# Kernel tuning notes

Measured on AMD Instinct MI355X. Metric: run time of the kernel, lower is better.

Reference implementation:

```python
import jax, jax.numpy as jnp
import numpy as np

N_NODES = 100000
N_EDGES = 1600000
IN_DIM = 128
HID_DIM = 128
OUT_DIM = 64


def gcn_conv(x, W, b, edge_index):
    """GCNConv with add_self_loops, symmetric degree norm, add-aggregation.

    Math matches PyG: out[i] = sum_{(j,i) in E+selfloops} norm_ji * (x_j @ W) + b
    Since lin is linear and there is no edge_attr, we transform x once before
    the gather instead of per-edge (identical result, far less FLOPs/traffic).
    """
    n = x.shape[0]
    loop = jnp.arange(n, dtype=edge_index.dtype)
    row = jnp.concatenate([edge_index[0], loop])  # source nodes (x_j)
    col = jnp.concatenate([edge_index[1], loop])  # destination nodes
    # degree over destinations (includes self loops -> deg >= 1, no div by 0)
    deg = jax.ops.segment_sum(jnp.ones_like(col, dtype=x.dtype), col, num_segments=n)
    dinv = jax.lax.rsqrt(deg)
    norm = dinv[row] * dinv[col]  # [E+N]
    h = x @ W  # [N, out] transform once
    msg = norm[:, None] * h[row]  # [E+N, out] gathered per-edge messages
    out = jax.ops.segment_sum(msg, col, num_segments=n)  # scatter-add
    return out + b


def setup_inputs() -> dict:
    key = jax.random.key(0)
    k1, k2, k3, k4 = jax.random.split(key, 4)
    x = jax.random.normal(k1, (N_NODES, IN_DIM), dtype=jnp.float32)
    edge_index = jax.random.randint(k2, (2, N_EDGES), 0, N_NODES, dtype=jnp.int64)
    # glorot-ish init
    W1 = jax.random.normal(k3, (IN_DIM, HID_DIM), dtype=jnp.float32) * (2.0 / (IN_DIM + HID_DIM)) ** 0.5
    W2 = jax.random.normal(k4, (HID_DIM, OUT_DIM), dtype=jnp.float32) * (2.0 / (HID_DIM + OUT_DIM)) ** 0.5
    b1 = jnp.zeros((HID_DIM,), dtype=jnp.float32)
    b2 = jnp.zeros((OUT_DIM,), dtype=jnp.float32)
    return {"x": x, "edge_index": edge_index, "W1": W1, "b1": b1, "W2": W2, "b2": b2}


def reference(x, edge_index, W1, b1, W2, b2):
    # GCN.forward with prompt_type=None, pooling=False, eval mode (dropout is identity)
    h = gcn_conv(x, W1, b1, edge_index)
    h = jax.nn.relu(h)
    out = gcn_conv(h, W2, b2, edge_index)
    return out
```

## Files before the change

### kernel.cpp

```cpp
#include <hip/hip_runtime.h>


#define DIN 128
#define DHID 128
#define DOUT 64
#define ELLW 64
#define GPART 8
#define BPG 512

typedef __attribute__((ext_vector_type(4))) float f32x4;
typedef __attribute__((ext_vector_type(8))) short bf16x8;

__device__ __forceinline__ float bf2f(unsigned int u16) {
    return __uint_as_float(u16 << 16);
}
__device__ __forceinline__ unsigned short f2bf(float f) {
    unsigned int u = __float_as_uint(f);
    u += 0x7fffu + ((u >> 16) & 1u);
    return (unsigned short)(u >> 16);
}
__device__ __forceinline__ unsigned int pack2(float a, float b) {
    return (unsigned int)f2bf(a) | ((unsigned int)f2bf(b) << 16);
}

__global__ __launch_bounds__(256) void k_packW(const float* __restrict__ W1,
                                               const float* __restrict__ W2,
                                               unsigned short* __restrict__ w1p,
                                               unsigned short* __restrict__ w2p,
                                               int* __restrict__ deg, int N) {
    int id = blockIdx.x * 256 + threadIdx.x;
    if (id < 2048) {
        int lane = id & 63, s = (id >> 6) & 3, t = id >> 8;
        int n = t * 16 + (lane & 15);
        int k0 = s * 32 + (lane >> 4) * 8;
#pragma unroll
        for (int j = 0; j < 8; ++j)
            w1p[(size_t)id * 8 + j] = f2bf(W1[(k0 + j) * DHID + n]);
    } else if (id < 3072) {
        int id2 = id - 2048;
        int lane = id2 & 63, s = (id2 >> 6) & 3, t = id2 >> 8;
        int n = t * 16 + (lane & 15);
        int k0 = s * 32 + (lane >> 4) * 8;
#pragma unroll
        for (int j = 0; j < 8; ++j)
            w2p[(size_t)id2 * 8 + j] = f2bf(W2[(k0 + j) * DOUT + n]);
    }
    for (int i = id; i < N; i += 12 * 256) deg[i] = 0;
}

__device__ __forceinline__ void fill_edge(int c, int r, int lo, int hi,
                                          int* __restrict__ deg, int* __restrict__ ell) {
    if (c >= lo && c < hi) {
        int k = atomicAdd(&deg[c], 1);
        if (k < ELLW) ell[(size_t)c * ELLW + k] = r;
    }
}

__global__ __launch_bounds__(256) void k_fill_gemm1(
        const int* __restrict__ rows, const int* __restrict__ cols,
        int* __restrict__ deg, int* __restrict__ ell,
        int E, int perBlock, int R, int GOCT, int GB,
        const float* __restrict__ x, const unsigned short* __restrict__ w1p,
        unsigned short* __restrict__ h1b, int N) {
    int bid = (int)blockIdx.x;
    int o = bid >> 3;
    int lane7 = bid & 7;
    int m = o / 3;
    int p = o - 3 * m;
    if (p == 2 && m < GOCT) {
        int gemmIdx = m * 8 + lane7;
        if (gemmIdx >= GB) return;
        int wave = threadIdx.x >> 6, lane = threadIdx.x & 63;
        int quad = lane >> 4, qr = lane & 15;
        int rowBase = gemmIdx * 64 + wave * 16;
        int arow = rowBase + qr;
        bool rowOK = arow < N;
        f32x4 acc[8] = {};
#pragma unroll
        for (int s = 0; s < 4; ++s) {
            bf16x8 a = {};
            if (rowOK) {
                const float* ap = x + (size_t)arow * DIN + s * 32 + quad * 8;
                float4 lo = *(const float4*)ap;
                float4 hi = *(const float4*)(ap + 4);
                a[0] = (short)f2bf(lo.x); a[1] = (short)f2bf(lo.y);
                a[2] = (short)f2bf(lo.z); a[3] = (short)f2bf(lo.w);
                a[4] = (short)f2bf(hi.x); a[5] = (short)f2bf(hi.y);
                a[6] = (short)f2bf(hi.z); a[7] = (short)f2bf(hi.w);
            }
#pragma unroll
            for (int t = 0; t < 8; ++t) {
                bf16x8 b = *(const bf16x8*)(w1p + ((size_t)(t * 4 + s) * 64 + lane) * 8);
                acc[t] = __builtin_amdgcn_mfma_f32_16x16x32_bf16(a, b, acc[t], 0, 0, 0);
            }
        }
#pragma unroll
        for (int t = 0; t < 8; ++t)
#pragma unroll
            for (int i = 0; i < 4; ++i) {
                int r = rowBase + quad * 4 + i;
                if (r < N) h1b[(size_t)r * DHID + t * 16 + qr] = f2bf(acc[t][i]);
            }
        return;
    }
    int gemBefore = (m < GOCT) ? m : GOCT;
    int chunk = o - gemBefore;
    int g = lane7;
    int lo = g * R, hi = lo + R;
    int eBeg = chunk * perBlock;
    int eEnd = eBeg + perBlock; if (eEnd > E) eEnd = E;
    for (int e = eBeg + 4 * threadIdx.x; e < eEnd; e += 4 * 256) {
        if (e + 3 < eEnd) {
            int4 c4 = *(const int4*)(cols + e);
            int4 r4 = *(const int4*)(rows + e);
            fill_edge(c4.x, r4.x, lo, hi, deg, ell);
            fill_edge(c4.y, r4.y, lo, hi, deg, ell);
            fill_edge(c4.z, r4.z, lo, hi, deg, ell);
            fill_edge(c4.w, r4.w, lo, hi, deg, ell);
        } else {
            for (int j = e; j < eEnd; ++j) fill_edge(cols[j], rows[j], lo, hi, deg, ell);
        }
    }
}

__global__ __launch_bounds__(256) void k_gather1g2(const int* __restrict__ deg,
                                                   const int* __restrict__ ell,
                                                   const uint2* __restrict__ h1v,
                                                   const float* __restrict__ b1,
                                                   const unsigned short* __restrict__ w2p,
                                                   unsigned short* __restrict__ h2b, int N) {
    __shared__ unsigned short hact_s[64][136];
    int wv = threadIdx.x >> 6;
    int lane = threadIdx.x & 63;
    int half = lane >> 5, col = lane & 31;
    int base = blockIdx.x * 64;
    float4 bv = *(const float4*)(b1 + 4 * col);
    for (int i = 0; i < 16; ++i) {
        int w = base + wv * 16 + i;
        if (w >= N) break;
        int d = deg[w]; if (d > ELLW) d = ELLW;
        int iv0 = ell[(size_t)w * ELLW + lane];
        int iv = (lane < d) ? iv0 : 0;
        float dv = (lane < d) ? rsqrtf((float)(deg[iv] + 1)) : 0.f;
        float a0 = 0.f, a1 = 0.f, a2 = 0.f, a3 = 0.f;
        int e = 0;
        for (; e + 16 <= d; e += 16) {
            int s[8]; float wg[8]; uint2 v[8];
#pragma unroll
            for (int j = 0; j < 8; ++j) {
                int idx = e + 2 * j + half;
                s[j] = __shfl(iv, idx); wg[j] = __shfl(dv, idx);
            }
#pragma unroll
            for (int j = 0; j < 8; ++j) v[j] = h1v[(size_t)s[j] * 32 + col];
#pragma unroll
            for (int j = 0; j < 8; ++j) {
                a0 = fmaf(wg[j], bf2f(v[j].x & 0xffffu), a0);
                a1 = fmaf(wg[j], bf2f(v[j].x >> 16), a1);
                a2 = fmaf(wg[j], bf2f(v[j].y & 0xffffu), a2);
                a3 = fmaf(wg[j], bf2f(v[j].y >> 16), a3);
            }
        }
        for (; e + 8 <= d; e += 8) {
            int s[4]; float wg[4]; uint2 v[4];
#pragma unroll
            for (int j = 0; j < 4; ++j) {
                int idx = e + 2 * j + half;
                s[j] = __shfl(iv, idx); wg[j] = __shfl(dv, idx);
            }
#pragma unroll
            for (int j = 0; j < 4; ++j) v[j] = h1v[(size_t)s[j] * 32 + col];
#pragma unroll
            for (int j = 0; j < 4; ++j) {
                a0 = fmaf(wg[j], bf2f(v[j].x & 0xffffu), a0);
                a1 = fmaf(wg[j], bf2f(v[j].x >> 16), a1);
                a2 = fmaf(wg[j], bf2f(v[j].y & 0xffffu), a2);
                a3 = fmaf(wg[j], bf2f(v[j].y >> 16), a3);
            }
        }
        for (; e < d; e += 2) {
            int idx = e + half;
            int s0 = __shfl(iv, idx); float w0 = __shfl(dv, idx);
            uint2 v0 = h1v[(size_t)s0 * 32 + col];
            a0 = fmaf(w0, bf2f(v0.x & 0xffffu), a0);
            a1 = fmaf(w0, bf2f(v0.x >> 16), a1);
            a2 = fmaf(w0, bf2f(v0.y & 0xffffu), a2);
            a3 = fmaf(w0, bf2f(v0.y >> 16), a3);
        }
        a0 += __shfl_xor(a0, 32); a1 += __shfl_xor(a1, 32);
        a2 += __shfl_xor(a2, 32); a3 += __shfl_xor(a3, 32);
        float di = rsqrtf((float)(d + 1)), self = di * di;
        uint2 hv = h1v[(size_t)w * 32 + col];
        float r0 = fmaf(di, a0, fmaf(self, bf2f(hv.x & 0xffffu), bv.x));
        float r1 = fmaf(di, a1, fmaf(self, bf2f(hv.x >> 16), bv.y));
        float r2 = fmaf(di, a2, fmaf(self, bf2f(hv.y & 0xffffu), bv.z));
        float r3 = fmaf(di, a3, fmaf(self, bf2f(hv.y >> 16), bv.w));
        if (lane < 32) {
            uint2 ov;
            ov.x = pack2(fmaxf(r0, 0.f), fmaxf(r1, 0.f));
            ov.y = pack2(fmaxf(r2, 0.f), fmaxf(r3, 0.f));
            *(uint2*)&hact_s[wv * 16 + i][4 * col] = ov;
        }
    }
    __syncthreads();
    int quad = lane >> 4, qr = lane & 15;
    int arow = wv * 16 + qr;
    f32x4 acc[4] = {};
#pragma unroll
    for (int s = 0; s < 4; ++s) {
        bf16x8 a = *(const bf16x8*)&hact_s[arow][s * 32 + quad * 8];
#pragma unroll
        for (int t = 0; t < 4; ++t) {
            bf16x8 b = *(const bf16x8*)(w2p + ((size_t)(t * 4 + s) * 64 + lane) * 8);
            acc[t] = __builtin_amdgcn_mfma_f32_16x16x32_bf16(a, b, acc[t], 0, 0, 0);
        }
    }
#pragma unroll
    for (int t = 0; t < 4; ++t)
#pragma unroll
        for (int i = 0; i < 4; ++i) {
            int r = base + wv * 16 + quad * 4 + i;
            if (r < N) h2b[(size_t)r * DOUT + t * 16 + qr] = f2bf(acc[t][i]);
        }
}

__global__ __launch_bounds__(256) void k_gather2(const int* __restrict__ deg,
                                                 const int* __restrict__ ell,
                                                 const unsigned int* __restrict__ h2v,
                                                 const float* __restrict__ b2,
                                                 float* __restrict__ out, int N) {
    int w = (blockIdx.x * 256 + threadIdx.x) >> 6;
    int lane = threadIdx.x & 63;
    if (w >= N) return;
    int d = deg[w]; if (d > ELLW) d = ELLW;
    int iv0 = ell[(size_t)w * ELLW + lane];
    int iv = (lane < d) ? iv0 : 0;
    float dv = (lane < d) ? rsqrtf((float)(deg[iv] + 1)) : 0.f;
    int half = lane >> 5, col = lane & 31;
    float a0 = 0.f, a1 = 0.f;
    int e = 0;
    for (; e + 16 <= d; e += 16) {
        int s[8]; float wg[8]; unsigned int v[8];
#pragma unroll
        for (int j = 0; j < 8; ++j) {
            int idx = e + 2 * j + half;
            s[j] = __shfl(iv, idx); wg[j] = __shfl(dv, idx);
        }
#pragma unroll
        for (int j = 0; j < 8; ++j) v[j] = h2v[(size_t)s[j] * 32 + col];
#pragma unroll
        for (int j = 0; j < 8; ++j) {
            a0 = fmaf(wg[j], bf2f(v[j] & 0xffffu), a0);
            a1 = fmaf(wg[j], bf2f(v[j] >> 16), a1);
        }
    }
    for (; e + 8 <= d; e += 8) {
        int s[4]; float wg[4]; unsigned int v[4];
#pragma unroll
        for (int j = 0; j < 4; ++j) {
            int idx = e + 2 * j + half;
            s[j] = __shfl(iv, idx); wg[j] = __shfl(dv, idx);
        }
#pragma unroll
        for (int j = 0; j < 4; ++j) v[j] = h2v[(size_t)s[j] * 32 + col];
#pragma unroll
        for (int j = 0; j < 4; ++j) {
            a0 = fmaf(wg[j], bf2f(v[j] & 0xffffu), a0);
            a1 = fmaf(wg[j], bf2f(v[j] >> 16), a1);
        }
    }
    for (; e < d; e += 2) {
        int idx = e + half;
        int s0 = __shfl(iv, idx); float w0 = __shfl(dv, idx);
        unsigned int v0 = h2v[(size_t)s0 * 32 + col];
        a0 = fmaf(w0, bf2f(v0 & 0xffffu), a0);
        a1 = fmaf(w0, bf2f(v0 >> 16), a1);
    }
    a0 += __shfl_xor(a0, 32); a1 += __shfl_xor(a1, 32);
    float di = rsqrtf((float)(d + 1)), self = di * di;
    unsigned int hv = h2v[(size_t)w * 32 + col];
    float2 bv = *(const float2*)(b2 + 2 * col);
    float r0 = fmaf(di, a0, fmaf(self, bf2f(hv & 0xffffu), bv.x));
    float r1 = fmaf(di, a1, fmaf(self, bf2f(hv >> 16), bv.y));
    if (lane < 32) {
        float2 ov; ov.x = r0; ov.y = r1;
        *(float2*)(out + (size_t)w * DOUT + 2 * col) = ov;
    }
}

extern "C" void kernel_launch(void* const* d_in, const int* in_sizes, int n_in,
                              void* d_out, int out_size, void* d_ws, size_t ws_size,
                              hipStream_t stream) {
    const float* x  = (const float*)d_in[0];
    const int*   ei = (const int*)d_in[1];
    const float* W1 = (const float*)d_in[2];
    const float* b1 = (const float*)d_in[3];
    const float* W2 = (const float*)d_in[4];
    const float* b2 = (const float*)d_in[5];

    const int N = in_sizes[0] / DIN;
    const int E = in_sizes[1] / 2;
    const int* rows = ei;
    const int* cols = ei + E;

    char* p = (char*)d_ws;
    int*   ell  = (int*)p;                    p += (size_t)N * ELLW * 4;
    unsigned short* h1b = (unsigned short*)p;   p += (size_t)N * DHID * 2;
    unsigned short* h2b = (unsigned short*)p;   p += (size_t)N * DOUT * 2;
    unsigned short* w1p = (unsigned short*)p;   p += (size_t)2048 * 8 * 2;
    unsigned short* w2p = (unsigned short*)p;   p += (size_t)1024 * 8 * 2;
    int*   deg  = (int*)p;                    p += (size_t)N * 4;

    const int R = (N + GPART - 1) / GPART;
    int perBlock = (E + BPG - 1) / BPG;
    perBlock = (perBlock + 3) & ~3;
    const int GB = (N + 63) / 64;
    const int GOCT = (GB + 7) / 8;
    const int OCT = BPG + GOCT;

    k_packW<<<12, 256, 0, stream>>>(W1, W2, w1p, w2p, deg, N);

    k_fill_gemm1<<<8 * OCT, 256, 0, stream>>>(rows, cols, deg, ell, E, perBlock, R,
                                              GOCT, GB, x, w1p, h1b, N);

    k_gather1g2<<<(N + 63) / 64, 256, 0, stream>>>(deg, ell, (const uint2*)h1b,
                                                   b1, w2p, h2b, N);

    k_gather2<<<(N + 3) / 4, 256, 0, stream>>>(deg, ell, (const unsigned int*)h2b,
                                               b2, (float*)d_out, N);
}
```

Baseline: 322.6 us.

## Shrink gather1 blocks to 16 nodes, split GEMM2 columns across waves, batch tails

The fused gather-plus-GEMM2 kernel now handles 16 nodes per block instead of 64. Each wave gathers 4 nodes, then computes one 16-column slice of the 16x64 output with MFMA. This gives four times more blocks, which should improve load balance and occupancy, at the cost of more block launches and syncs. Both gather kernels also replace the serial 2-edge remainder loop with one masked 4-wide batch, skip ELL index loads for lanes beyond the degree, and zero-fill shared rows for out-of-range nodes.

```diff
diff --git a/kernel.cpp b/kernel.cpp
--- a/kernel.cpp
+++ b/kernel.cpp
@@ -129,99 +129,109 @@
                                                    const float* __restrict__ b1,
                                                    const unsigned short* __restrict__ w2p,
                                                    unsigned short* __restrict__ h2b, int N) {
-    __shared__ unsigned short hact_s[64][136];
+    __shared__ unsigned short hact_s[16][136];
     int wv = threadIdx.x >> 6;
     int lane = threadIdx.x & 63;
     int half = lane >> 5, col = lane & 31;
-    int base = blockIdx.x * 64;
+    int base = blockIdx.x * 16;
     float4 bv = *(const float4*)(b1 + 4 * col);
-    for (int i = 0; i < 16; ++i) {
-        int w = base + wv * 16 + i;
-        if (w >= N) break;
-        int d = deg[w]; if (d > ELLW) d = ELLW;
-        int iv0 = ell[(size_t)w * ELLW + lane];
-        int iv = (lane < d) ? iv0 : 0;
-        float dv = (lane < d) ? rsqrtf((float)(deg[iv] + 1)) : 0.f;
-        float a0 = 0.f, a1 = 0.f, a2 = 0.f, a3 = 0.f;
-        int e = 0;
-        for (; e + 16 <= d; e += 16) {
-            int s[8]; float wg[8]; uint2 v[8];
-#pragma unroll
-            for (int j = 0; j < 8; ++j) {
-                int idx = e + 2 * j + half;
-                s[j] = __shfl(iv, idx); wg[j] = __shfl(dv, idx);
-            }
-#pragma unroll
-            for (int j = 0; j < 8; ++j) v[j] = h1v[(size_t)s[j] * 32 + col];
-#pragma unroll
-            for (int j = 0; j < 8; ++j) {
-                a0 = fmaf(wg[j], bf2f(v[j].x & 0xffffu), a0);
-                a1 = fmaf(wg[j], bf2f(v[j].x >> 16), a1);
-                a2 = fmaf(wg[j], bf2f(v[j].y & 0xffffu), a2);
-                a3 = fmaf(wg[j], bf2f(v[j].y >> 16), a3);
-            }
-        }
-        for (; e + 8 <= d; e += 8) {
-            int s[4]; float wg[4]; uint2 v[4];
-#pragma unroll
-            for (int j = 0; j < 4; ++j) {
-                int idx = e + 2 * j + half;
-                s[j] = __shfl(iv, idx); wg[j] = __shfl(dv, idx);
-            }
-#pragma unroll
-            for (int j = 0; j < 4; ++j) v[j] = h1v[(size_t)s[j] * 32 + col];
-#pragma unroll
-            for (int j = 0; j < 4; ++j) {
-                a0 = fmaf(wg[j], bf2f(v[j].x & 0xffffu), a0);
-                a1 = fmaf(wg[j], bf2f(v[j].x >> 16), a1);
-                a2 = fmaf(wg[j], bf2f(v[j].y & 0xffffu), a2);
-                a3 = fmaf(wg[j], bf2f(v[j].y >> 16), a3);
-            }
-        }
-        for (; e < d; e += 2) {
-            int idx = e + half;
-            int s0 = __shfl(iv, idx); float w0 = __shfl(dv, idx);
-            uint2 v0 = h1v[(size_t)s0 * 32 + col];
-            a0 = fmaf(w0, bf2f(v0.x & 0xffffu), a0);
-            a1 = fmaf(w0, bf2f(v0.x >> 16), a1);
-            a2 = fmaf(w0, bf2f(v0.y & 0xffffu), a2);
-            a3 = fmaf(w0, bf2f(v0.y >> 16), a3);
-        }
-        a0 += __shfl_xor(a0, 32); a1 += __shfl_xor(a1, 32);
-        a2 += __shfl_xor(a2, 32); a3 += __shfl_xor(a3, 32);
-        float di = rsqrtf((float)(d + 1)), self = di * di;
-        uint2 hv = h1v[(size_t)w * 32 + col];
-        float r0 = fmaf(di, a0, fmaf(self, bf2f(hv.x & 0xffffu), bv.x));
-        float r1 = fmaf(di, a1, fmaf(self, bf2f(hv.x >> 16), bv.y));
-        float r2 = fmaf(di, a2, fmaf(self, bf2f(hv.y & 0xffffu), bv.z));
-        float r3 = fmaf(di, a3, fmaf(self, bf2f(hv.y >> 16), bv.w));
-        if (lane < 32) {
-            uint2 ov;
-            ov.x = pack2(fmaxf(r0, 0.f), fmaxf(r1, 0.f));
-            ov.y = pack2(fmaxf(r2, 0.f), fmaxf(r3, 0.f));
-            *(uint2*)&hact_s[wv * 16 + i][4 * col] = ov;
+    for (int i = 0; i < 4; ++i) {
+        int w = base + wv * 4 + i;
+        if (w < N) {
+            int d = deg[w]; if (d > ELLW) d = ELLW;
+            int iv = 0;
+            if (lane < d) iv = ell[(size_t)w * ELLW + lane];
+            float dv = (lane < d) ? rsqrtf((float)(deg[iv] + 1)) : 0.f;
+            float a0 = 0.f, a1 = 0.f, a2 = 0.f, a3 = 0.f;
+            int e = 0;
+            for (; e + 16 <= d; e += 16) {
+                int s[8]; float wg[8]; uint2 v[8];
+#pragma unroll
+                for (int j = 0; j < 8; ++j) {
+                    int idx = e + 2 * j + half;
+                    s[j] = __shfl(iv, idx); wg[j] = __shfl(dv, idx);
+                }
+#pragma unroll
+                for (int j = 0; j < 8; ++j) v[j] = h1v[(size_t)s[j] * 32 + col];
+#pragma unroll
+                for (int j = 0; j < 8; ++j) {
+                    a0 = fmaf(wg[j], bf2f(v[j].x & 0xffffu), a0);
+                    a1 = fmaf(wg[j], bf2f(v[j].x >> 16), a1);
+                    a2 = fmaf(wg[j], bf2f(v[j].y & 0xffffu), a2);
+                    a3 = fmaf(wg[j], bf2f(v[j].y >> 16), a3);
+                }
+            }
+            if (e + 8 <= d) {
+                int s[4]; float wg[4]; uint2 v[4];
+#pragma unroll
+                for (int j = 0; j < 4; ++j) {
+                    int idx = e + 2 * j + half;
+                    s[j] = __shfl(iv, idx); wg[j] = __shfl(dv, idx);
+                }
+#pragma unroll
+                for (int j = 0; j < 4; ++j) v[j] = h1v[(size_t)s[j] * 32 + col];
+#pragma unroll
+                for (int j = 0; j < 4; ++j) {
+                    a0 = fmaf(wg[j], bf2f(v[j].x & 0xffffu), a0);
+                    a1 = fmaf(wg[j], bf2f(v[j].x >> 16), a1);
+                    a2 = fmaf(wg[j], bf2f(v[j].y & 0xffffu), a2);
+                    a3 = fmaf(wg[j], bf2f(v[j].y >> 16), a3);
+                }
+                e += 8;
+            }
+            if (e < d) {
+                int s[4]; float wg[4]; uint2 v[4];
+#pragma unroll
+                for (int j = 0; j < 4; ++j) {
+                    int idx = e + 2 * j + half;
+                    int cl = idx < 63 ? idx : 63;
+                    s[j] = __shfl(iv, cl);
+                    float t = __shfl(dv, cl);
+                    wg[j] = (idx < d) ? t : 0.f;
+                }
+#pragma unroll
+                for (int j = 0; j < 4; ++j) v[j] = h1v[(size_t)s[j] * 32 + col];
+#pragma unroll
+                for (int j = 0; j < 4; ++j) {
+                    a0 = fmaf(wg[j], bf2f(v[j].x & 0xffffu), a0);
+                    a1 = fmaf(wg[j], bf2f(v[j].x >> 16), a1);
+                    a2 = fmaf(wg[j], bf2f(v[j].y & 0xffffu), a2);
+                    a3 = fmaf(wg[j], bf2f(v[j].y >> 16), a3);
+                }
+            }
+            a0 += __shfl_xor(a0, 32); a1 += __shfl_xor(a1, 32);
+            a2 += __shfl_xor(a2, 32); a3 += __shfl_xor(a3, 32);
+            float di = rsqrtf((float)(d + 1)), self = di * di;
+            uint2 hv = h1v[(size_t)w * 32 + col];
+            float r0 = fmaf(di, a0, fmaf(self, bf2f(hv.x & 0xffffu), bv.x));
+            float r1 = fmaf(di, a1, fmaf(self, bf2f(hv.x >> 16), bv.y));
+            float r2 = fmaf(di, a2, fmaf(self, bf2f(hv.y & 0xffffu), bv.z));
+            float r3 = fmaf(di, a3, fmaf(self, bf2f(hv.y >> 16), bv.w));
+            if (lane < 32) {
+                uint2 ov;
+                ov.x = pack2(fmaxf(r0, 0.f), fmaxf(r1, 0.f));
+                ov.y = pack2(fmaxf(r2, 0.f), fmaxf(r3, 0.f));
+                *(uint2*)&hact_s[wv * 4 + i][4 * col] = ov;
+            }
+        } else if (lane < 32) {
+            uint2 z; z.x = 0u; z.y = 0u;
+            *(uint2*)&hact_s[wv * 4 + i][4 * col] = z;
         }
     }
     __syncthreads();
     int quad = lane >> 4, qr = lane & 15;
-    int arow = wv * 16 + qr;
-    f32x4 acc[4] = {};
+    f32x4 acc = {};
 #pragma unroll
     for (int s = 0; s < 4; ++s) {
-        bf16x8 a = *(const bf16x8*)&hact_s[arow][s * 32 + quad * 8];
-#pragma unroll
-        for (int t = 0; t < 4; ++t) {
-            bf16x8 b = *(const bf16x8*)(w2p + ((size_t)(t * 4 + s) * 64 + lane) * 8);
-            acc[t] = __builtin_amdgcn_mfma_f32_16x16x32_bf16(a, b, acc[t], 0, 0, 0);
-        }
-    }
-#pragma unroll
-    for (int t = 0; t < 4; ++t)
-#pragma unroll
-        for (int i = 0; i < 4; ++i) {
-            int r = base + wv * 16 + quad * 4 + i;
-            if (r < N) h2b[(size_t)r * DOUT + t * 16 + qr] = f2bf(acc[t][i]);
-        }
+        bf16x8 a = *(const bf16x8*)&hact_s[qr][s * 32 + quad * 8];
+        bf16x8 b = *(const bf16x8*)(w2p + ((size_t)(wv * 4 + s) * 64 + lane) * 8);
+        acc = __builtin_amdgcn_mfma_f32_16x16x32_bf16(a, b, acc, 0, 0, 0);
+    }
+#pragma unroll
+    for (int i = 0; i < 4; ++i) {
+        int r = base + quad * 4 + i;
+        if (r < N) h2b[(size_t)r * DOUT + wv * 16 + qr] = f2bf(acc[i]);
+    }
 }
 
 __global__ __launch_bounds__(256) void k_gather2(const int* __restrict__ deg,
@@ -233,8 +243,8 @@
     int lane = threadIdx.x & 63;
     if (w >= N) return;
     int d = deg[w]; if (d > ELLW) d = ELLW;
-    int iv0 = ell[(size_t)w * ELLW + lane];
-    int iv = (lane < d) ? iv0 : 0;
+    int iv = 0;
+    if (lane < d) iv = ell[(size_t)w * ELLW + lane];
     float dv = (lane < d) ? rsqrtf((float)(deg[iv] + 1)) : 0.f;
     int half = lane >> 5, col = lane & 31;
     float a0 = 0.f, a1 = 0.f;
@@ -254,7 +264,7 @@
             a1 = fmaf(wg[j], bf2f(v[j] >> 16), a1);
         }
     }
-    for (; e + 8 <= d; e += 8) {
+    if (e + 8 <= d) {
         int s[4]; float wg[4]; unsigned int v[4];
 #pragma unroll
         for (int j = 0; j < 4; ++j) {
@@ -268,13 +278,25 @@
             a0 = fmaf(wg[j], bf2f(v[j] & 0xffffu), a0);
             a1 = fmaf(wg[j], bf2f(v[j] >> 16), a1);
         }
-    }
-    for (; e < d; e += 2) {
-        int idx = e + half;
-        int s0 = __shfl(iv, idx); float w0 = __shfl(dv, idx);
-        unsigned int v0 = h2v[(size_t)s0 * 32 + col];
-        a0 = fmaf(w0, bf2f(v0 & 0xffffu), a0);
-        a1 = fmaf(w0, bf2f(v0 >> 16), a1);
+        e += 8;
+    }
+    if (e < d) {
+        int s[4]; float wg[4]; unsigned int v[4];
+#pragma unroll
+        for (int j = 0; j < 4; ++j) {
+            int idx = e + 2 * j + half;
+            int cl = idx < 63 ? idx : 63;
+            s[j] = __shfl(iv, cl);
+            float t = __shfl(dv, cl);
+            wg[j] = (idx < d) ? t : 0.f;
+        }
+#pragma unroll
+        for (int j = 0; j < 4; ++j) v[j] = h2v[(size_t)s[j] * 32 + col];
+#pragma unroll
+        for (int j = 0; j < 4; ++j) {
+            a0 = fmaf(wg[j], bf2f(v[j] & 0xffffu), a0);
+            a1 = fmaf(wg[j], bf2f(v[j] >> 16), a1);
+        }
     }
     a0 += __shfl_xor(a0, 32); a1 += __shfl_xor(a1, 32);
     float di = rsqrtf((float)(d + 1)), self = di * di;
@@ -323,7 +345,7 @@
     k_fill_gemm1<<<8 * OCT, 256, 0, stream>>>(rows, cols, deg, ell, E, perBlock, R,
                                               GOCT, GB, x, w1p, h1b, N);
 
-    k_gather1g2<<<(N + 63) / 64, 256, 0, stream>>>(deg, ell, (const uint2*)h1b,
+    k_gather1g2<<<(N + 15) / 16, 256, 0, stream>>>(deg, ell, (const uint2*)h1b,
                                                    b1, w2p, h2b, N);
 
     k_gather2<<<(N + 3) / 4, 256, 0, stream>>>(deg, ell, (const unsigned int*)h2b,
```

Result: faster. 295.9 us, median of 2 (-8.3%).
